# Optimization experiments

Hardware: AMD Instinct MI355X
Metric: run time of the kernel (lower is better)

Reference implementation:

```python
import jax, jax.numpy as jnp
import numpy as np

NEG_SLOPE = 0.2  # PyG GATConv leaky_relu slope
N_NODE = 1000   # nodes per graph (= n_nodes ctor arg = lstm1 input_size)
BATCH = 32      # num_graphs
C = 32          # in_channels == GAT out_channels per head
HEADS = 8
E = 384000      # total edges over the batched graph
H1, H2 = 32, 128
N_PRED = 2
N = N_NODE * BATCH


def _lstm(x_seq, W_ih, W_hh, b_ih, b_hh):
    # x_seq: [T, B, In]; PyTorch gate order i,f,g,o
    B = x_seq.shape[1]
    Hd = W_hh.shape[1]
    h0 = jnp.zeros((B, Hd), x_seq.dtype)

    def step(carry, x_t):
        h, c = carry
        g = x_t @ W_ih.T + h @ W_hh.T + b_ih + b_hh
        i, f, gg, o = jnp.split(g, 4, axis=-1)
        c = jax.nn.sigmoid(f) * c + jax.nn.sigmoid(i) * jnp.tanh(gg)
        h = jax.nn.sigmoid(o) * jnp.tanh(c)
        return (h, c), h

    (_, _), hs = jax.lax.scan(step, (h0, h0), x_seq)
    return hs


def setup_inputs() -> dict:
    key = jax.random.key(0)
    ks = jax.random.split(key, 20)
    inp = {}
    inp["x"] = jax.random.normal(ks[0], (N, C), jnp.float32)
    inp["src"] = jax.random.randint(ks[1], (E,), 0, N)
    inp["dst"] = jax.random.randint(ks[2], (E,), 0, N)
    inp["batch_size"] = BATCH
    # GATConv params (concat=False: mean over heads)
    inp["W_gat"] = jax.random.normal(ks[3], (C, HEADS * C), jnp.float32) * 0.1
    inp["a_src"] = jax.random.normal(ks[4], (HEADS, C), jnp.float32) * 0.1
    inp["a_dst"] = jax.random.normal(ks[5], (HEADS, C), jnp.float32) * 0.1
    inp["b_gat"] = jnp.zeros((C,), jnp.float32)
    # LSTM1: input N_NODE -> hidden 32
    inp["W_ih1"] = jax.random.normal(ks[6], (4 * H1, N_NODE), jnp.float32) * 0.05
    inp["W_hh1"] = jax.random.normal(ks[7], (4 * H1, H1), jnp.float32) * 0.1
    inp["b_ih1"] = jnp.zeros((4 * H1,), jnp.float32)
    inp["b_hh1"] = jnp.zeros((4 * H1,), jnp.float32)
    # LSTM2: input 32 -> hidden 128 (repaired from buggy source)
    inp["W_ih2"] = jax.random.normal(ks[8], (4 * H2, H1), jnp.float32) * 0.1
    inp["W_hh2"] = jax.random.normal(ks[9], (4 * H2, H2), jnp.float32) * 0.08
    inp["b_ih2"] = jnp.zeros((4 * H2,), jnp.float32)
    inp["b_hh2"] = jnp.zeros((4 * H2,), jnp.float32)
    # Linear head: 128 -> n_nodes * n_pred
    inp["W_lin"] = jax.random.normal(ks[10], (N_NODE * N_PRED, H2), jnp.float32) * 0.08
    inp["b_lin"] = jnp.zeros((N_NODE * N_PRED,), jnp.float32)
    return inp


def reference(x, src, dst, batch_size, W_gat, a_src, a_dst, b_gat,
              W_ih1, W_hh1, b_ih1, b_hh1, W_ih2, W_hh2, b_ih2, b_hh2,
              W_lin, b_lin):
    n, c = x.shape
    h = a_src.shape[0]
    # --- GATConv ---
    x_lin = (x @ W_gat).reshape(n, h, c)               # [N, H, C]
    asrc = jnp.einsum('nhc,hc->nh', x_lin, a_src)      # [N, H]
    adst = jnp.einsum('nhc,hc->nh', x_lin, a_dst)
    e = jax.nn.leaky_relu(asrc[src] + adst[dst], NEG_SLOPE)   # [E, H]
    m = jax.ops.segment_max(e, dst, num_segments=n)
    m = jnp.where(jnp.isfinite(m), m, 0.0)             # isolated nodes
    ew = jnp.exp(e - m[dst])
    denom = jax.ops.segment_sum(ew, dst, num_segments=n)
    alpha = ew / jnp.maximum(denom[dst], 1e-16)        # segment softmax
    agg = jax.ops.segment_sum(alpha[:, :, None] * x_lin[src], dst, num_segments=n)
    out = agg.mean(axis=1) + b_gat                     # concat=False -> head mean; [N, C]
    # --- reshape: seq over feature dim, LSTM input = nodes-per-graph ---
    n_node = n // batch_size
    seq = jnp.moveaxis(out.reshape(batch_size, n_node, c), 2, 0)  # [C, B, n_node]
    h1 = _lstm(seq, W_ih1, W_hh1, b_ih1, b_hh1)
    h2 = _lstm(h1, W_ih2, W_hh2, b_ih2, b_hh2)
    last = h2[-1]                                       # [B, 128]
    y = last @ W_lin.T + b_lin                          # [B, n_node*n_pred]
    return y.reshape(batch_size * n_node, -1)           # [B*n_node, n_pred]
```

## Files before the change

kernel.cpp:

```cpp
#include <hip/hip_runtime.h>
#include <hip/hip_fp16.h>
#include <math.h>

#define NEG_SLOPE 0.2f

__device__ __forceinline__ float sigm(float x) { return 1.0f / (1.0f + __expf(-x)); }
__device__ __forceinline__ float tanh_fast(float x) {
    float xc = fminf(fmaxf(x, -15.0f), 15.0f);
    float e2 = __expf(2.0f * xc);
    return (e2 - 1.0f) / (e2 + 1.0f);
}
__device__ __forceinline__ float lrelu(float x) { return (x > 0.0f) ? x : NEG_SLOPE * x; }

typedef _Float16 h2v __attribute__((ext_vector_type(2)));
__device__ __forceinline__ float fdot2h(h2v a, h2v b, float c) {
#if __has_builtin(__builtin_amdgcn_fdot2)
    return __builtin_amdgcn_fdot2(a, b, c, false);
#else
    return (float)a[0] * (float)b[0] + (float)a[1] * (float)b[1] + c;
#endif
}

__global__ void k_zero(int* __restrict__ deg, int N) {
    int i = blockIdx.x * 256 + threadIdx.x;
    if (i < N) deg[i] = 0;
}

__global__ void k_hist(const int* __restrict__ dst, int* __restrict__ deg, int E) {
    int e = blockIdx.x * 256 + threadIdx.x;
    if (e < E) atomicAdd(deg + dst[e], 1);
}

__global__ __launch_bounds__(256) void k_scan1(const int* __restrict__ deg,
                                               int* __restrict__ blksum, int N) {
    __shared__ int s[256];
    int tid = threadIdx.x;
    int i = blockIdx.x * 256 + tid;
    int v = (i < N) ? deg[i] : 0;
    s[tid] = v;
    __syncthreads();
    #pragma unroll
    for (int off = 128; off > 0; off >>= 1) {
        if (tid < off) s[tid] += s[tid + off];
        __syncthreads();
    }
    if (tid == 0) blksum[blockIdx.x] = s[0];
}

__global__ __launch_bounds__(256) void k_scan2(const int* __restrict__ blksum,
                                               int* __restrict__ blkoff, int nb) {
    __shared__ int s[256];
    int tid = threadIdx.x;
    int v = (tid < nb) ? blksum[tid] : 0;
    s[tid] = v;
    __syncthreads();
    for (int off = 1; off < 256; off <<= 1) {
        int t = (tid >= off) ? s[tid - off] : 0;
        __syncthreads();
        s[tid] += t;
        __syncthreads();
    }
    if (tid < nb) blkoff[tid] = s[tid] - v;
}

__global__ __launch_bounds__(256) void k_scan3(const int* __restrict__ deg,
                                               const int* __restrict__ blkoff,
                                               int* __restrict__ rowptr,
                                               int* __restrict__ cursor, int N, int E) {
    __shared__ int s[256];
    int tid = threadIdx.x;
    int i = blockIdx.x * 256 + tid;
    int v = (i < N) ? deg[i] : 0;
    s[tid] = v;
    __syncthreads();
    for (int off = 1; off < 256; off <<= 1) {
        int t = (tid >= off) ? s[tid - off] : 0;
        __syncthreads();
        s[tid] += t;
        __syncthreads();
    }
    int excl = s[tid] - v + blkoff[blockIdx.x];
    if (i < N) { rowptr[i] = excl; cursor[i] = excl; }
    if (i == N - 1) rowptr[N] = E;
}

__global__ void k_scatter(const int* __restrict__ src, const int* __restrict__ dst,
                          int* __restrict__ cursor, int* __restrict__ csr_src, int E) {
    int e = blockIdx.x * 256 + threadIdx.x;
    if (e < E) {
        int pos = atomicAdd(cursor + dst[e], 1);
        csr_src[pos] = src[e];
    }
}

__global__ void k_pre(const float* __restrict__ W_gat, const float* __restrict__ a_src,
                      const float* __restrict__ a_dst, float* __restrict__ wa) {
    int tid = threadIdx.x;
    int k = tid >> 3, h = tid & 7;
    float s1 = 0.0f, s2 = 0.0f;
    for (int c = 0; c < 32; ++c) {
        float wv = W_gat[k * 256 + h * 32 + c];
        s1 += wv * a_src[h * 32 + c];
        s2 += wv * a_dst[h * 32 + c];
    }
    wa[tid] = s1;
    wa[256 + tid] = s2;
}

__global__ __launch_bounds__(256) void k_att(const float* __restrict__ x,
                                             const float* __restrict__ wa,
                                             float* __restrict__ asrc,
                                             float* __restrict__ adst) {
    __shared__ float xs[32 * 33];
    __shared__ float was[256], wad[256];
    int tid = threadIdx.x;
    int n0 = blockIdx.x * 32;
    for (int i = tid; i < 1024; i += 256) {
        int nl = i >> 5, k = i & 31;
        xs[nl * 33 + k] = x[(size_t)(n0 + nl) * 32 + k];
    }
    was[tid] = wa[tid];
    wad[tid] = wa[256 + tid];
    __syncthreads();
    int nl = tid >> 3, h = tid & 7;
    float s1 = 0.0f, s2 = 0.0f;
    #pragma unroll
    for (int k = 0; k < 32; ++k) {
        float xv = xs[nl * 33 + k];
        s1 += xv * was[k * 8 + h];
        s2 += xv * wad[k * 8 + h];
    }
    asrc[(size_t)(n0 + nl) * 8 + h] = s1;
    adst[(size_t)(n0 + nl) * 8 + h] = s2;
}

__global__ __launch_bounds__(256) void k_gat(
    const int* __restrict__ rowptr, const int* __restrict__ csr_src,
    const float* __restrict__ asrc, const float* __restrict__ adst,
    const float* __restrict__ x, float* __restrict__ z, int N) {
    int w = (blockIdx.x * 256 + threadIdx.x) >> 6;
    int lane = threadIdx.x & 63;
    if (w >= N) return;
    int r0 = rowptr[w], r1 = rowptr[w + 1];
    int h = lane >> 3, kq = lane & 7;
    float ad = adst[w * 8 + h];
    float4 acc = make_float4(0.0f, 0.0f, 0.0f, 0.0f);
    float den = 0.0f;
    const float4* x4 = (const float4*)x;
    for (int i = r0; i < r1; ++i) {
        int s = csr_src[i];
        float ew = __expf(lrelu(asrc[s * 8 + h] + ad));
        float4 xv = x4[(size_t)s * 8 + kq];
        acc.x += ew * xv.x; acc.y += ew * xv.y;
        acc.z += ew * xv.z; acc.w += ew * xv.w;
        den += ew;
    }
    float inv = 1.0f / fmaxf(den, 1e-16f);
    float4 r = make_float4(acc.x * inv, acc.y * inv, acc.z * inv, acc.w * inv);
    ((float4*)z)[(size_t)w * 64 + lane] = r;
}

__global__ __launch_bounds__(256) void k_zw(
    const float* __restrict__ z, const float* __restrict__ W_gat,
    const float* __restrict__ b_gat, float* __restrict__ gatT, int N, int n_node) {
    int gw = (blockIdx.x * 256 + threadIdx.x) >> 6;
    int lane = threadIdx.x & 63;
    int chalf = gw & 1;
    int nset = gw >> 1;
    int c = chalf * 16 + (lane & 15);
    int sl = lane >> 4;
    float wcol[64];
    #pragma unroll
    for (int i = 0; i < 64; ++i) {
        int k = i & 31, hh = sl * 2 + (i >> 5);
        wcol[i] = 0.125f * W_gat[k * 256 + hh * 32 + c];
    }
    float bg = b_gat[c];
    const float4* z4 = (const float4*)z;
    for (int it = 0; it < 8; ++it) {
        int n = nset * 8 + it;
        if (n >= N) break;
        float p = 0.0f;
        #pragma unroll
        for (int k4 = 0; k4 < 16; ++k4) {
            float4 zv = z4[(size_t)n * 64 + sl * 16 + k4];
            p += zv.x * wcol[4 * k4] + zv.y * wcol[4 * k4 + 1]
               + zv.z * wcol[4 * k4 + 2] + zv.w * wcol[4 * k4 + 3];
        }
        p += __shfl_xor(p, 16, 64);
        p += __shfl_xor(p, 32, 64);
        if (lane < 16) {
            int b = n / n_node, kk = n - b * n_node;
            gatT[((size_t)b * 32 + c) * n_node + kk] = p + bg;
        }
    }
}

__global__ __launch_bounds__(256) void k_wt(const float* __restrict__ W,
                                            float* __restrict__ Wt, int n_node) {
    __shared__ float tle[32][33];
    int kt = blockIdx.x & 31;
    int gt = blockIdx.x >> 5;
    int tid = threadIdx.x;
    for (int i = tid; i < 1024; i += 256) {
        int gl = i >> 5, kl = i & 31;
        int g = gt * 32 + gl, k = kt * 32 + kl;
        tle[gl][kl] = (k < n_node) ? W[(size_t)g * n_node + k] : 0.0f;
    }
    __syncthreads();
    for (int i = tid; i < 1024; i += 256) {
        int kl = i >> 5, gl = i & 31;
        int k = kt * 32 + kl, g = gt * 32 + gl;
        if (k < n_node) Wt[(size_t)k * 128 + g] = tle[gl][kl];
    }
}

__global__ __launch_bounds__(256) void k_p1(
    const float* __restrict__ gatT, const float* __restrict__ Wt,
    const float* __restrict__ b_ih1, const float* __restrict__ b_hh1,
    float* __restrict__ P1, int n_node, int B) {
    __shared__ __align__(16) float Arow[2][1024];
    __shared__ __align__(16) float part[4][2][128];
    int blk = blockIdx.x;
    int b = blk >> 4;
    int tq = blk & 15;
    int tid = threadIdx.x;
    const float* A0 = gatT + ((size_t)b * 32 + tq * 2) * n_node;
    #pragma unroll
    for (int r = 0; r < 2; ++r)
        for (int i = tid; i < n_node; i += 256)
            Arow[r][i] = A0[(size_t)r * n_node + i];
    __syncthreads();

    int g4 = tid & 31;
    int tloc = (tid >> 5) & 1;
    int ks = tid >> 6;
    int kq = n_node >> 2;
    int k0 = ks * kq;
    const float4* Wt4 = (const float4*)Wt;
    float4 acc = make_float4(0.0f, 0.0f, 0.0f, 0.0f);
    #pragma unroll 4
    for (int k = 0; k < kq; ++k) {
        float4 w = Wt4[(size_t)(k0 + k) * 32 + g4];
        float a = Arow[tloc][k0 + k];
        acc.x += w.x * a; acc.y += w.y * a;
        acc.z += w.z * a; acc.w += w.w * a;
    }
    *(float4*)&part[ks][tloc][g4 * 4] = acc;
    __syncthreads();

    int tl = tid >> 7, g = tid & 127;
    float s = part[0][tl][g] + part[1][tl][g] + part[2][tl][g] + part[3][tl][g]
            + b_ih1[g] + b_hh1[g];
    int t = tq * 2 + tl;
    P1[((size_t)t * B + b) * 128 + g] = s;
}

__global__ __launch_bounds__(640) void k_lstm(
    const float* __restrict__ P1, const float* __restrict__ W_hh1,
    const float* __restrict__ W_ih2, const float* __restrict__ W_hh2,
    const float* __restrict__ b_ih2, const float* __restrict__ b_hh2,
    float* __restrict__ h2finT, int B, int T) {
    __shared__ __align__(16) float P1s[32][128];
    __shared__ __align__(16) float h1s[32];
    __shared__ __align__(16) float g1s[128];
    __shared__ __align__(16) float h1all[32][32];
    __shared__ __align__(16) __half hbuf[2][128];
    int tid = threadIdx.x, b = blockIdx.x;

    for (int i = tid; i < 4096; i += 640) {
        int t = i >> 7, g = i & 127;
        P1s[t][g] = P1[((size_t)t * B + b) * 128 + g];
    }

    float4 w1[8];
    if (tid < 128) {
        const float4* W = (const float4*)(W_hh1 + (size_t)tid * 32);
        #pragma unroll
        for (int j = 0; j < 8; ++j) w1[j] = W[j];
    }

    int tid2 = tid - 128;
    int gt = tid2 & 3, n = tid2 >> 2;
    int g_idx = gt * 128 + n;
    h2v wh[64];
    float4 wi[8];
    float bias = 0.0f;
    if (tid >= 128) {
        const float4* Wr = (const float4*)(W_hh2 + (size_t)g_idx * 128);
        #pragma unroll
        for (int j = 0; j < 32; ++j) {
            float4 w = Wr[j];
            h2v t0, t1;
            t0[0] = (_Float16)w.x; t0[1] = (_Float16)w.y;
            t1[0] = (_Float16)w.z; t1[1] = (_Float16)w.w;
            wh[2 * j] = t0;
            wh[2 * j + 1] = t1;
        }
        const float4* Wi = (const float4*)(W_ih2 + (size_t)g_idx * 32);
        #pragma unroll
        for (int j = 0; j < 8; ++j) wi[j] = Wi[j];
        bias = b_ih2[g_idx] + b_hh2[g_idx];
    }

    if (tid < 32) h1s[tid] = 0.0f;
    if (tid >= 128 && tid < 256) hbuf[0][tid - 128] = __float2half(0.0f);
    float c1 = 0.0f, c2 = 0.0f;
    __syncthreads();

    for (int s = 0; s <= T; ++s) {
        if (tid < 128) {
            if (s < T) {
                float acc = P1s[s][tid];
                const float4* hp = (const float4*)h1s;
                #pragma unroll
                for (int j = 0; j < 8; ++j) {
                    float4 h = hp[j], w = w1[j];
                    acc += w.x * h.x + w.y * h.y + w.z * h.z + w.w * h.w;
                }
                g1s[tid] = acc;
            }
        } else if (s >= 1) {
            int t2 = s - 1;
            const float4* hp1 = (const float4*)h1all[t2];
            float p = bias;
            #pragma unroll
            for (int j = 0; j < 8; ++j) {
                float4 w = wi[j], h = hp1[j];
                p += w.x * h.x + w.y * h.y + w.z * h.z + w.w * h.w;
            }
            const uint4* hc4 = (const uint4*)hbuf[t2 & 1];
            float a0 = 0.0f, a1 = 0.0f, a2 = 0.0f, a3 = 0.0f;
            #pragma unroll
            for (int j = 0; j < 16; ++j) {
                uint4 hv = hc4[j];
                const h2v* hp = reinterpret_cast<const h2v*>(&hv);
                a0 = fdot2h(wh[4 * j],     hp[0], a0);
                a1 = fdot2h(wh[4 * j + 1], hp[1], a1);
                a2 = fdot2h(wh[4 * j + 2], hp[2], a2);
                a3 = fdot2h(wh[4 * j + 3], hp[3], a3);
            }
            float acc = p + ((a0 + a1) + (a2 + a3));
            float v1 = __shfl_xor(acc, 1, 64);
            float v2 = __shfl_xor(acc, 2, 64);
            float v3 = __shfl_xor(acc, 3, 64);
            if (gt == 0) {
                float i_ = sigm(acc), f_ = sigm(v1);
                float g_ = tanh_fast(v2), o_ = sigm(v3);
                c2 = f_ * c2 + i_ * g_;
                float h = o_ * tanh_fast(c2);
                hbuf[(t2 + 1) & 1][n] = __float2half(h);
                if (t2 == T - 1) h2finT[n * 32 + b] = h;
            }
        }
        __syncthreads();
        if (tid < 32 && s < T) {
            float i_ = sigm(g1s[tid]), f_ = sigm(g1s[32 + tid]);
            float g_ = tanh_fast(g1s[64 + tid]), o_ = sigm(g1s[96 + tid]);
            c1 = f_ * c1 + i_ * g_;
            float h = o_ * tanh_fast(c1);
            h1s[tid] = h;
            h1all[s][tid] = h;
        }
        __syncthreads();
    }
}

__global__ __launch_bounds__(256) void k_fin(
    const float* __restrict__ h2finT, const float* __restrict__ W_lin,
    const float* __restrict__ b_lin, float* __restrict__ out, int n_node, int B) {
    __shared__ __align__(16) float hs[128];
    int b = blockIdx.x >> 3;
    int kc = blockIdx.x & 7;
    int tid = threadIdx.x;
    if (tid < 128) hs[tid] = h2finT[tid * 32 + b];
    __syncthreads();
    int outdim = n_node * 2;
    int kk = kc * 256 + tid;
    if (kk < outdim) {
        float acc = b_lin[kk];
        const float4* W4 = (const float4*)(W_lin + (size_t)kk * 128);
        const float4* h4 = (const float4*)hs;
        #pragma unroll 8
        for (int j = 0; j < 32; ++j) {
            float4 w = W4[j], h = h4[j];
            acc += w.x * h.x + w.y * h.y + w.z * h.z + w.w * h.w;
        }
        out[(size_t)b * outdim + kk] = acc;
    }
}

extern "C" void kernel_launch(void* const* d_in, const int* in_sizes, int n_in,
                              void* d_out, int out_size, void* d_ws, size_t ws_size,
                              hipStream_t stream) {
    const float* x     = (const float*)d_in[0];
    const int*   src   = (const int*)d_in[1];
    const int*   dst   = (const int*)d_in[2];
    const float* W_gat = (const float*)d_in[4];
    const float* a_src = (const float*)d_in[5];
    const float* a_dst = (const float*)d_in[6];
    const float* b_gat = (const float*)d_in[7];
    const float* W_ih1 = (const float*)d_in[8];
    const float* W_hh1 = (const float*)d_in[9];
    const float* b_ih1 = (const float*)d_in[10];
    const float* b_hh1 = (const float*)d_in[11];
    const float* W_ih2 = (const float*)d_in[12];
    const float* W_hh2 = (const float*)d_in[13];
    const float* b_ih2 = (const float*)d_in[14];
    const float* b_hh2 = (const float*)d_in[15];
    const float* W_lin = (const float*)d_in[16];
    const float* b_lin = (const float*)d_in[17];

    int N = in_sizes[0] / 32;
    int E = in_sizes[1];
    int n_node = in_sizes[8] / 128;
    int B = N / n_node;
    int T = 32;

    float* ws = (float*)d_ws;
    float* z      = ws;
    float* asrc   = z + (size_t)N * 256;
    float* adst   = asrc + (size_t)N * 8;
    float* gatT   = adst + (size_t)N * 8;
    float* P1     = gatT + (size_t)N * 32;
    float* h1g    = P1 + (size_t)T * B * 128;
    float* P2g    = h1g + (size_t)B * 1024;
    float* h2finT = P2g + (size_t)B * 16384;
    float* wa     = h2finT + 128 * 32;
    int* deg     = (int*)(wa + 512);
    int* cursor  = deg + N;
    int* rowptr  = cursor + N;
    int* csr_src = rowptr + N + 1;
    int* blksum  = csr_src + E;
    int* blkoff  = blksum + 256;
    float* Wt    = (float*)(((uintptr_t)(blkoff + 256) + 255) & ~(uintptr_t)255);

    int nb = (N + 255) / 256;

    k_wt<<<128, 256, 0, stream>>>(W_ih1, Wt, n_node);
    k_zero<<<(N + 255) / 256, 256, 0, stream>>>(deg, N);
    k_hist<<<(E + 255) / 256, 256, 0, stream>>>(dst, deg, E);
    k_scan1<<<nb, 256, 0, stream>>>(deg, blksum, N);
    k_scan2<<<1, 256, 0, stream>>>(blksum, blkoff, nb);
    k_scan3<<<nb, 256, 0, stream>>>(deg, blkoff, rowptr, cursor, N, E);
    k_scatter<<<(E + 255) / 256, 256, 0, stream>>>(src, dst, cursor, csr_src, E);
    k_pre<<<1, 256, 0, stream>>>(W_gat, a_src, a_dst, wa);
    k_att<<<N / 32, 256, 0, stream>>>(x, wa, asrc, adst);
    k_gat<<<(N * 64 + 255) / 256, 256, 0, stream>>>(rowptr, csr_src, asrc, adst,
                                                    x, z, N);
    k_zw<<<2000, 256, 0, stream>>>(z, W_gat, b_gat, gatT, N, n_node);
    k_p1<<<B * 16, 256, 0, stream>>>(gatT, Wt, b_ih1, b_hh1, P1, n_node, B);
    k_lstm<<<B, 640, 0, stream>>>(P1, W_hh1, W_ih2, W_hh2, b_ih2, b_hh2,
                                  h2finT, B, T);
    k_fin<<<B * 8, 256, 0, stream>>>(h2finT, W_lin, b_lin, (float*)d_out, n_node, B);
}
```

Measured before the change: 239.8 us.

## Fuse LSTM1 gate activation via shuffles, drop a barrier, prepack LSTM2 weights

Reorders LSTM1 gate rows so each group of four lanes holds the i/f/g/o gates of one hidden unit. The cell update is then done with lane shuffles instead of a shared-memory round trip, which removes one __syncthreads per time step and double-buffers h1. LSTM2 recurrent weights are converted to fp16 and packed in a coalesced layout by a new pre-kernel, so the LSTM kernel's weight loads are coalesced and need no conversion. The dot-product loop uses eight accumulators, and launch bounds now request 3 blocks per SM, which may constrain register allocation.

Result: faster. 228.3 us (-4.8%).

```diff
diff --git a/kernel.cpp b/kernel.cpp
--- a/kernel.cpp
+++ b/kernel.cpp
@@ -215,6 +215,23 @@
     }
 }
 
+__global__ __launch_bounds__(256) void k_pack2(
+    const float* __restrict__ W_hh2, const float* __restrict__ W_ih2,
+    uint4* __restrict__ wpack, float4* __restrict__ wipack) {
+    int i = blockIdx.x * 256 + threadIdx.x;
+    int j = i >> 9, t2 = i & 511;
+    int g = (t2 & 3) * 128 + (t2 >> 2);
+    const float* p = W_hh2 + (size_t)g * 128 + j * 8;
+    __align__(16) _Float16 tmp[8];
+    #pragma unroll
+    for (int k = 0; k < 8; ++k) tmp[k] = (_Float16)p[k];
+    wpack[j * 512 + t2] = *(const uint4*)tmp;
+    if (j < 8) {
+        const float4* q = (const float4*)(W_ih2 + (size_t)g * 32) + j;
+        wipack[j * 512 + t2] = *q;
+    }
+}
+
 __global__ __launch_bounds__(256) void k_p1(
     const float* __restrict__ gatT, const float* __restrict__ Wt,
     const float* __restrict__ b_ih1, const float* __restrict__ b_hh1,
@@ -256,14 +273,13 @@
     P1[((size_t)t * B + b) * 128 + g] = s;
 }
 
-__global__ __launch_bounds__(640) void k_lstm(
+__global__ __launch_bounds__(640, 3) void k_lstm(
     const float* __restrict__ P1, const float* __restrict__ W_hh1,
-    const float* __restrict__ W_ih2, const float* __restrict__ W_hh2,
+    const uint4* __restrict__ wpack, const float4* __restrict__ wipack,
     const float* __restrict__ b_ih2, const float* __restrict__ b_hh2,
     float* __restrict__ h2finT, int B, int T) {
     __shared__ __align__(16) float P1s[32][128];
-    __shared__ __align__(16) float h1s[32];
-    __shared__ __align__(16) float g1s[128];
+    __shared__ __align__(16) float h1d[2][32];
     __shared__ __align__(16) float h1all[32][32];
     __shared__ __align__(16) __half hbuf[2][128];
     int tid = threadIdx.x, b = blockIdx.x;
@@ -273,9 +289,12 @@
         P1s[t][g] = P1[((size_t)t * B + b) * 128 + g];
     }
 
+    int n1 = (tid >> 2) & 31, gt1 = tid & 3;
+    int r1 = gt1 * 32 + n1;
     float4 w1[8];
+    float c1 = 0.0f;
     if (tid < 128) {
-        const float4* W = (const float4*)(W_hh1 + (size_t)tid * 32);
+        const float4* W = (const float4*)(W_hh1 + (size_t)r1 * 32);
         #pragma unroll
         for (int j = 0; j < 8; ++j) w1[j] = W[j];
     }
@@ -283,64 +302,72 @@
     int tid2 = tid - 128;
     int gt = tid2 & 3, n = tid2 >> 2;
     int g_idx = gt * 128 + n;
-    h2v wh[64];
+    uint4 whq[16];
     float4 wi[8];
-    float bias = 0.0f;
+    float bias = 0.0f, c2 = 0.0f;
     if (tid >= 128) {
-        const float4* Wr = (const float4*)(W_hh2 + (size_t)g_idx * 128);
         #pragma unroll
-        for (int j = 0; j < 32; ++j) {
-            float4 w = Wr[j];
-            h2v t0, t1;
-            t0[0] = (_Float16)w.x; t0[1] = (_Float16)w.y;
-            t1[0] = (_Float16)w.z; t1[1] = (_Float16)w.w;
-            wh[2 * j] = t0;
-            wh[2 * j + 1] = t1;
-        }
-        const float4* Wi = (const float4*)(W_ih2 + (size_t)g_idx * 32);
+        for (int j = 0; j < 16; ++j) whq[j] = wpack[j * 512 + tid2];
         #pragma unroll
-        for (int j = 0; j < 8; ++j) wi[j] = Wi[j];
+        for (int j = 0; j < 8; ++j) wi[j] = wipack[j * 512 + tid2];
         bias = b_ih2[g_idx] + b_hh2[g_idx];
     }
 
-    if (tid < 32) h1s[tid] = 0.0f;
+    if (tid < 32) h1d[0][tid] = 0.0f;
     if (tid >= 128 && tid < 256) hbuf[0][tid - 128] = __float2half(0.0f);
-    float c1 = 0.0f, c2 = 0.0f;
     __syncthreads();
 
     for (int s = 0; s <= T; ++s) {
         if (tid < 128) {
             if (s < T) {
-                float acc = P1s[s][tid];
-                const float4* hp = (const float4*)h1s;
+                float acc = P1s[s][r1];
+                const float4* hp = (const float4*)h1d[s & 1];
                 #pragma unroll
                 for (int j = 0; j < 8; ++j) {
                     float4 h = hp[j], w = w1[j];
                     acc += w.x * h.x + w.y * h.y + w.z * h.z + w.w * h.w;
                 }
-                g1s[tid] = acc;
+                float v1 = __shfl_xor(acc, 1, 64);
+                float v2 = __shfl_xor(acc, 2, 64);
+                float v3 = __shfl_xor(acc, 3, 64);
+                if (gt1 == 0) {
+                    float i_ = sigm(acc), f_ = sigm(v1);
+                    float g_ = tanh_fast(v2), o_ = sigm(v3);
+                    c1 = f_ * c1 + i_ * g_;
+                    float h = o_ * tanh_fast(c1);
+                    h1d[(s + 1) & 1][n1] = h;
+                    h1all[s][n1] = h;
+                }
             }
         } else if (s >= 1) {
-            int t2 = s - 1;
-            const float4* hp1 = (const float4*)h1all[t2];
+            int t2s = s - 1;
+            const float4* hp1 = (const float4*)h1all[t2s];
             float p = bias;
             #pragma unroll
             for (int j = 0; j < 8; ++j) {
                 float4 w = wi[j], h = hp1[j];
                 p += w.x * h.x + w.y * h.y + w.z * h.z + w.w * h.w;
             }
-            const uint4* hc4 = (const uint4*)hbuf[t2 & 1];
+            const uint4* hc4 = (const uint4*)hbuf[t2s & 1];
             float a0 = 0.0f, a1 = 0.0f, a2 = 0.0f, a3 = 0.0f;
+            float a4 = 0.0f, a5 = 0.0f, a6 = 0.0f, a7 = 0.0f;
             #pragma unroll
-            for (int j = 0; j < 16; ++j) {
-                uint4 hv = hc4[j];
-                const h2v* hp = reinterpret_cast<const h2v*>(&hv);
-                a0 = fdot2h(wh[4 * j],     hp[0], a0);
-                a1 = fdot2h(wh[4 * j + 1], hp[1], a1);
-                a2 = fdot2h(wh[4 * j + 2], hp[2], a2);
-                a3 = fdot2h(wh[4 * j + 3], hp[3], a3);
+            for (int j = 0; j < 16; j += 2) {
+                uint4 hvA = hc4[j], hvB = hc4[j + 1];
+                const h2v* ha = reinterpret_cast<const h2v*>(&hvA);
+                const h2v* hb = reinterpret_cast<const h2v*>(&hvB);
+                const h2v* wa_ = reinterpret_cast<const h2v*>(&whq[j]);
+                const h2v* wb_ = reinterpret_cast<const h2v*>(&whq[j + 1]);
+                a0 = fdot2h(wa_[0], ha[0], a0);
+                a1 = fdot2h(wa_[1], ha[1], a1);
+                a2 = fdot2h(wa_[2], ha[2], a2);
+                a3 = fdot2h(wa_[3], ha[3], a3);
+                a4 = fdot2h(wb_[0], hb[0], a4);
+                a5 = fdot2h(wb_[1], hb[1], a5);
+                a6 = fdot2h(wb_[2], hb[2], a6);
+                a7 = fdot2h(wb_[3], hb[3], a7);
             }
-            float acc = p + ((a0 + a1) + (a2 + a3));
+            float acc = p + (((a0 + a1) + (a2 + a3)) + ((a4 + a5) + (a6 + a7)));
             float v1 = __shfl_xor(acc, 1, 64);
             float v2 = __shfl_xor(acc, 2, 64);
             float v3 = __shfl_xor(acc, 3, 64);
@@ -349,18 +376,9 @@
                 float g_ = tanh_fast(v2), o_ = sigm(v3);
                 c2 = f_ * c2 + i_ * g_;
                 float h = o_ * tanh_fast(c2);
-                hbuf[(t2 + 1) & 1][n] = __float2half(h);
-                if (t2 == T - 1) h2finT[n * 32 + b] = h;
+                hbuf[(t2s + 1) & 1][n] = __float2half(h);
+                if (t2s == T - 1) h2finT[n * 32 + b] = h;
             }
-        }
-        __syncthreads();
-        if (tid < 32 && s < T) {
-            float i_ = sigm(g1s[tid]), f_ = sigm(g1s[32 + tid]);
-            float g_ = tanh_fast(g1s[64 + tid]), o_ = sigm(g1s[96 + tid]);
-            c1 = f_ * c1 + i_ * g_;
-            float h = o_ * tanh_fast(c1);
-            h1s[tid] = h;
-            h1all[s][tid] = h;
         }
         __syncthreads();
     }
@@ -423,9 +441,9 @@
     float* adst   = asrc + (size_t)N * 8;
     float* gatT   = adst + (size_t)N * 8;
     float* P1     = gatT + (size_t)N * 32;
-    float* h1g    = P1 + (size_t)T * B * 128;
-    float* P2g    = h1g + (size_t)B * 1024;
-    float* h2finT = P2g + (size_t)B * 16384;
+    float* wpackf = P1 + (size_t)T * B * 128;
+    float* wipackf= wpackf + 32768;
+    float* h2finT = wipackf + 16384;
     float* wa     = h2finT + 128 * 32;
     int* deg     = (int*)(wa + 512);
     int* cursor  = deg + N;
@@ -435,8 +453,12 @@
     int* blkoff  = blksum + 256;
     float* Wt    = (float*)(((uintptr_t)(blkoff + 256) + 255) & ~(uintptr_t)255);
 
+    uint4*  wpack  = (uint4*)wpackf;
+    float4* wipack = (float4*)wipackf;
+
     int nb = (N + 255) / 256;
 
+    k_pack2<<<32, 256, 0, stream>>>(W_hh2, W_ih2, wpack, wipack);
     k_wt<<<128, 256, 0, stream>>>(W_ih1, Wt, n_node);
     k_zero<<<(N + 255) / 256, 256, 0, stream>>>(deg, N);
     k_hist<<<(E + 255) / 256, 256, 0, stream>>>(dst, deg, E);
@@ -450,7 +472,7 @@
                                                     x, z, N);
     k_zw<<<2000, 256, 0, stream>>>(z, W_gat, b_gat, gatT, N, n_node);
     k_p1<<<B * 16, 256, 0, stream>>>(gatT, Wt, b_ih1, b_hh1, P1, n_node, B);
-    k_lstm<<<B, 640, 0, stream>>>(P1, W_hh1, W_ih2, W_hh2, b_ih2, b_hh2,
+    k_lstm<<<B, 640, 0, stream>>>(P1, W_hh1, wpack, wipack, b_ih2, b_hh2,
                                   h2finT, B, T);
     k_fin<<<B * 8, 256, 0, stream>>>(h2finT, W_lin, b_lin, (float*)d_out, n_node, B);
 }
```

## Restructure fused LSTM kernel to 1024 threads with split-K gate dot products

Applied to the files above, without the earlier changes.

The fused two-layer LSTM kernel now uses 1024 threads per batch. Eight threads split each hidden unit's recurrent dot product and combine partial sums with shuffles, instead of one thread per gate holding a full fp16 weight row. A new pre-pack kernel converts and reorders W_hh2, W_ih2 and W_hh1 into coalesced per-thread layouts. Layer 1 now uses shuffles for its gates and double-buffered h1, which removes one barrier per timestep, and layer 2 runs concurrently one step behind. The aim is to shorten the serial per-step latency of the recurrence, at the cost of an extra launch and more shuffle work.

After: 240.7 us. About the same (+0.4%).

```diff
diff --git a/kernel.cpp b/kernel.cpp
--- a/kernel.cpp
+++ b/kernel.cpp
@@ -215,6 +215,33 @@
     }
 }
 
+__global__ __launch_bounds__(256) void k_pack2(
+    const float* __restrict__ W_hh2, const float* __restrict__ W_ih2,
+    const float* __restrict__ W_hh1,
+    uint4* __restrict__ wc2, float4* __restrict__ wif4, float4* __restrict__ w1f4) {
+    int i = blockIdx.x * 256 + threadIdx.x;
+    if (i < 8192) {
+        int j = i >> 10, t = i & 1023;
+        int n = t >> 3, q = t & 7;
+        int g = j >> 1, jj = j & 1;
+        const float* p = W_hh2 + (size_t)(g * 128 + n) * 128 + q * 16 + jj * 8;
+        __align__(16) _Float16 tmp[8];
+        #pragma unroll
+        for (int k = 0; k < 8; ++k) tmp[k] = (_Float16)p[k];
+        wc2[j * 1024 + t] = *(const uint4*)tmp;
+    } else if (i < 12288) {
+        int ii = i - 8192;
+        int j = ii >> 10, t = ii & 1023;
+        int n = t >> 3, q = t & 7;
+        wif4[j * 1024 + t] = *(const float4*)(W_ih2 + (size_t)(j * 128 + n) * 32 + q * 4);
+    } else if (i < 13312) {
+        int ii = i - 12288;
+        int j = ii >> 7, t1 = ii & 127;
+        int r1 = (t1 & 3) * 32 + (t1 >> 2);
+        w1f4[j * 128 + t1] = *(const float4*)(W_hh1 + (size_t)r1 * 32 + j * 4);
+    }
+}
+
 __global__ __launch_bounds__(256) void k_p1(
     const float* __restrict__ gatT, const float* __restrict__ Wt,
     const float* __restrict__ b_ih1, const float* __restrict__ b_hh1,
@@ -256,111 +283,129 @@
     P1[((size_t)t * B + b) * 128 + g] = s;
 }
 
-__global__ __launch_bounds__(640) void k_lstm(
-    const float* __restrict__ P1, const float* __restrict__ W_hh1,
-    const float* __restrict__ W_ih2, const float* __restrict__ W_hh2,
+__attribute__((amdgpu_waves_per_eu(4, 4)))
+__global__ __launch_bounds__(1024) void k_lstm(
+    const float* __restrict__ P1, const uint4* __restrict__ wc2,
+    const float4* __restrict__ wif4, const float4* __restrict__ w1f4,
     const float* __restrict__ b_ih2, const float* __restrict__ b_hh2,
     float* __restrict__ h2finT, int B, int T) {
     __shared__ __align__(16) float P1s[32][128];
-    __shared__ __align__(16) float h1s[32];
-    __shared__ __align__(16) float g1s[128];
-    __shared__ __align__(16) float h1all[32][32];
+    __shared__ __align__(16) float h1d[2][32];
     __shared__ __align__(16) __half hbuf[2][128];
     int tid = threadIdx.x, b = blockIdx.x;
-
-    for (int i = tid; i < 4096; i += 640) {
-        int t = i >> 7, g = i & 127;
-        P1s[t][g] = P1[((size_t)t * B + b) * 128 + g];
-    }
-
+    int n = tid >> 3, q = tid & 7;
+
+    for (int i = tid; i < 4096; i += 1024)
+        P1s[i >> 7][i & 127] = P1[((size_t)(i >> 7) * B + b) * 128 + (i & 127)];
+
+    uint4 wc[8];
+    #pragma unroll
+    for (int j = 0; j < 8; ++j) wc[j] = wc2[j * 1024 + tid];
+    float4 wi0 = wif4[tid];
+    float4 wi1 = wif4[1024 + tid];
+    float4 wi2 = wif4[2048 + tid];
+    float4 wi3 = wif4[3072 + tid];
+    float bias0 = b_ih2[n] + b_hh2[n];
+    float bias1 = b_ih2[128 + n] + b_hh2[128 + n];
+    float bias2 = b_ih2[256 + n] + b_hh2[256 + n];
+    float bias3 = b_ih2[384 + n] + b_hh2[384 + n];
+
+    int gt1 = tid & 3;
+    int r1 = gt1 * 32 + (tid >> 2);
     float4 w1[8];
     if (tid < 128) {
-        const float4* W = (const float4*)(W_hh1 + (size_t)tid * 32);
         #pragma unroll
-        for (int j = 0; j < 8; ++j) w1[j] = W[j];
-    }
-
-    int tid2 = tid - 128;
-    int gt = tid2 & 3, n = tid2 >> 2;
-    int g_idx = gt * 128 + n;
-    h2v wh[64];
-    float4 wi[8];
-    float bias = 0.0f;
-    if (tid >= 128) {
-        const float4* Wr = (const float4*)(W_hh2 + (size_t)g_idx * 128);
-        #pragma unroll
-        for (int j = 0; j < 32; ++j) {
-            float4 w = Wr[j];
-            h2v t0, t1;
-            t0[0] = (_Float16)w.x; t0[1] = (_Float16)w.y;
-            t1[0] = (_Float16)w.z; t1[1] = (_Float16)w.w;
-            wh[2 * j] = t0;
-            wh[2 * j + 1] = t1;
-        }
-        const float4* Wi = (const float4*)(W_ih2 + (size_t)g_idx * 32);
-        #pragma unroll
-        for (int j = 0; j < 8; ++j) wi[j] = Wi[j];
-        bias = b_ih2[g_idx] + b_hh2[g_idx];
-    }
-
-    if (tid < 32) h1s[tid] = 0.0f;
-    if (tid >= 128 && tid < 256) hbuf[0][tid - 128] = __float2half(0.0f);
+        for (int j = 0; j < 8; ++j) w1[j] = w1f4[j * 128 + tid];
+    }
+    if (tid < 32) h1d[0][tid] = 0.0f;
+    if (tid < 128) hbuf[0][tid] = __float2half(0.0f);
     float c1 = 0.0f, c2 = 0.0f;
     __syncthreads();
 
     for (int s = 0; s <= T; ++s) {
-        if (tid < 128) {
-            if (s < T) {
-                float acc = P1s[s][tid];
-                const float4* hp = (const float4*)h1s;
-                #pragma unroll
-                for (int j = 0; j < 8; ++j) {
-                    float4 h = hp[j], w = w1[j];
-                    acc += w.x * h.x + w.y * h.y + w.z * h.z + w.w * h.w;
-                }
-                g1s[tid] = acc;
-            }
-        } else if (s >= 1) {
+        if (s >= 1) {
             int t2 = s - 1;
-            const float4* hp1 = (const float4*)h1all[t2];
-            float p = bias;
-            #pragma unroll
-            for (int j = 0; j < 8; ++j) {
-                float4 w = wi[j], h = hp1[j];
-                p += w.x * h.x + w.y * h.y + w.z * h.z + w.w * h.w;
-            }
-            const uint4* hc4 = (const uint4*)hbuf[t2 & 1];
-            float a0 = 0.0f, a1 = 0.0f, a2 = 0.0f, a3 = 0.0f;
-            #pragma unroll
-            for (int j = 0; j < 16; ++j) {
-                uint4 hv = hc4[j];
-                const h2v* hp = reinterpret_cast<const h2v*>(&hv);
-                a0 = fdot2h(wh[4 * j],     hp[0], a0);
-                a1 = fdot2h(wh[4 * j + 1], hp[1], a1);
-                a2 = fdot2h(wh[4 * j + 2], hp[2], a2);
-                a3 = fdot2h(wh[4 * j + 3], hp[3], a3);
-            }
-            float acc = p + ((a0 + a1) + (a2 + a3));
-            float v1 = __shfl_xor(acc, 1, 64);
-            float v2 = __shfl_xor(acc, 2, 64);
-            float v3 = __shfl_xor(acc, 3, 64);
-            if (gt == 0) {
-                float i_ = sigm(acc), f_ = sigm(v1);
-                float g_ = tanh_fast(v2), o_ = sigm(v3);
+            const uint4* hb = (const uint4*)hbuf[t2 & 1];
+            uint4 h2a = hb[q * 2];
+            uint4 h2b = hb[q * 2 + 1];
+            float4 h1v = ((const float4*)h1d[s & 1])[q];
+            const h2v* ha = reinterpret_cast<const h2v*>(&h2a);
+            const h2v* hc = reinterpret_cast<const h2v*>(&h2b);
+            float sg0 = wi0.x * h1v.x + wi0.y * h1v.y + wi0.z * h1v.z + wi0.w * h1v.w;
+            float sg1 = wi1.x * h1v.x + wi1.y * h1v.y + wi1.z * h1v.z + wi1.w * h1v.w;
+            float sg2 = wi2.x * h1v.x + wi2.y * h1v.y + wi2.z * h1v.z + wi2.w * h1v.w;
+            float sg3 = wi3.x * h1v.x + wi3.y * h1v.y + wi3.z * h1v.z + wi3.w * h1v.w;
+            {
+                const h2v* wa_ = reinterpret_cast<const h2v*>(&wc[0]);
+                const h2v* wb_ = reinterpret_cast<const h2v*>(&wc[1]);
+                float a0 = 0, a1 = 0, a2 = 0, a3 = 0;
+                a0 = fdot2h(wa_[0], ha[0], a0); a1 = fdot2h(wa_[1], ha[1], a1);
+                a2 = fdot2h(wa_[2], ha[2], a2); a3 = fdot2h(wa_[3], ha[3], a3);
+                a0 = fdot2h(wb_[0], hc[0], a0); a1 = fdot2h(wb_[1], hc[1], a1);
+                a2 = fdot2h(wb_[2], hc[2], a2); a3 = fdot2h(wb_[3], hc[3], a3);
+                sg0 += (a0 + a1) + (a2 + a3);
+            }
+            {
+                const h2v* wa_ = reinterpret_cast<const h2v*>(&wc[2]);
+                const h2v* wb_ = reinterpret_cast<const h2v*>(&wc[3]);
+                float a0 = 0, a1 = 0, a2 = 0, a3 = 0;
+                a0 = fdot2h(wa_[0], ha[0], a0); a1 = fdot2h(wa_[1], ha[1], a1);
+                a2 = fdot2h(wa_[2], ha[2], a2); a3 = fdot2h(wa_[3], ha[3], a3);
+                a0 = fdot2h(wb_[0], hc[0], a0); a1 = fdot2h(wb_[1], hc[1], a1);
+                a2 = fdot2h(wb_[2], hc[2], a2); a3 = fdot2h(wb_[3], hc[3], a3);
+                sg1 += (a0 + a1) + (a2 + a3);
+            }
+            {
+                const h2v* wa_ = reinterpret_cast<const h2v*>(&wc[4]);
+                const h2v* wb_ = reinterpret_cast<const h2v*>(&wc[5]);
+                float a0 = 0, a1 = 0, a2 = 0, a3 = 0;
+                a0 = fdot2h(wa_[0], ha[0], a0); a1 = fdot2h(wa_[1], ha[1], a1);
+                a2 = fdot2h(wa_[2], ha[2], a2); a3 = fdot2h(wa_[3], ha[3], a3);
+                a0 = fdot2h(wb_[0], hc[0], a0); a1 = fdot2h(wb_[1], hc[1], a1);
+                a2 = fdot2h(wb_[2], hc[2], a2); a3 = fdot2h(wb_[3], hc[3], a3);
+                sg2 += (a0 + a1) + (a2 + a3);
+            }
+            {
+                const h2v* wa_ = reinterpret_cast<const h2v*>(&wc[6]);
+                const h2v* wb_ = reinterpret_cast<const h2v*>(&wc[7]);
+                float a0 = 0, a1 = 0, a2 = 0, a3 = 0;
+                a0 = fdot2h(wa_[0], ha[0], a0); a1 = fdot2h(wa_[1], ha[1], a1);
+                a2 = fdot2h(wa_[2], ha[2], a2); a3 = fdot2h(wa_[3], ha[3], a3);
+                a0 = fdot2h(wb_[0], hc[0], a0); a1 = fdot2h(wb_[1], hc[1], a1);
+                a2 = fdot2h(wb_[2], hc[2], a2); a3 = fdot2h(wb_[3], hc[3], a3);
+                sg3 += (a0 + a1) + (a2 + a3);
+            }
+            sg0 += __shfl_xor(sg0, 1, 64); sg0 += __shfl_xor(sg0, 2, 64); sg0 += __shfl_xor(sg0, 4, 64);
+            sg1 += __shfl_xor(sg1, 1, 64); sg1 += __shfl_xor(sg1, 2, 64); sg1 += __shfl_xor(sg1, 4, 64);
+            sg2 += __shfl_xor(sg2, 1, 64); sg2 += __shfl_xor(sg2, 2, 64); sg2 += __shfl_xor(sg2, 4, 64);
+            sg3 += __shfl_xor(sg3, 1, 64); sg3 += __shfl_xor(sg3, 2, 64); sg3 += __shfl_xor(sg3, 4, 64);
+            if (q == 0) {
+                float i_ = sigm(sg0 + bias0), f_ = sigm(sg1 + bias1);
+                float g_ = tanh_fast(sg2 + bias2), o_ = sigm(sg3 + bias3);
                 c2 = f_ * c2 + i_ * g_;
                 float h = o_ * tanh_fast(c2);
                 hbuf[(t2 + 1) & 1][n] = __float2half(h);
                 if (t2 == T - 1) h2finT[n * 32 + b] = h;
             }
         }
-        __syncthreads();
-        if (tid < 32 && s < T) {
-            float i_ = sigm(g1s[tid]), f_ = sigm(g1s[32 + tid]);
-            float g_ = tanh_fast(g1s[64 + tid]), o_ = sigm(g1s[96 + tid]);
-            c1 = f_ * c1 + i_ * g_;
-            float h = o_ * tanh_fast(c1);
-            h1s[tid] = h;
-            h1all[s][tid] = h;
+        if (tid < 128 && s < T) {
+            const float4* hp = (const float4*)h1d[s & 1];
+            float acc = P1s[s][r1];
+            #pragma unroll
+            for (int j = 0; j < 8; ++j) {
+                float4 h = hp[j], w = w1[j];
+                acc += w.x * h.x + w.y * h.y + w.z * h.z + w.w * h.w;
+            }
+            float v1 = __shfl_xor(acc, 1, 64);
+            float v2 = __shfl_xor(acc, 2, 64);
+            float v3 = __shfl_xor(acc, 3, 64);
+            if (gt1 == 0) {
+                float i_ = sigm(acc), f_ = sigm(v1);
+                float g_ = tanh_fast(v2), o_ = sigm(v3);
+                c1 = f_ * c1 + i_ * g_;
+                float h = o_ * tanh_fast(c1);
+                h1d[(s + 1) & 1][tid >> 2] = h;
+            }
         }
         __syncthreads();
     }
@@ -423,9 +468,10 @@
     float* adst   = asrc + (size_t)N * 8;
     float* gatT   = adst + (size_t)N * 8;
     float* P1     = gatT + (size_t)N * 32;
-    float* h1g    = P1 + (size_t)T * B * 128;
-    float* P2g    = h1g + (size_t)B * 1024;
-    float* h2finT = P2g + (size_t)B * 16384;
+    float* wc2f   = P1 + (size_t)T * B * 128;
+    float* wiff   = wc2f + 32768;
+    float* w1ff   = wiff + 16384;
+    float* h2finT = w1ff + 4096;
     float* wa     = h2finT + 128 * 32;
     int* deg     = (int*)(wa + 512);
     int* cursor  = deg + N;
@@ -435,8 +481,13 @@
     int* blkoff  = blksum + 256;
     float* Wt    = (float*)(((uintptr_t)(blkoff + 256) + 255) & ~(uintptr_t)255);
 
+    uint4*  wc2  = (uint4*)wc2f;
+    float4* wif4 = (float4*)wiff;
+    float4* w1f4 = (float4*)w1ff;
+
     int nb = (N + 255) / 256;
 
+    k_pack2<<<52, 256, 0, stream>>>(W_hh2, W_ih2, W_hh1, wc2, wif4, w1f4);
     k_wt<<<128, 256, 0, stream>>>(W_ih1, Wt, n_node);
     k_zero<<<(N + 255) / 256, 256, 0, stream>>>(deg, N);
     k_hist<<<(E + 255) / 256, 256, 0, stream>>>(dst, deg, E);
@@ -450,7 +501,6 @@
                                                     x, z, N);
     k_zw<<<2000, 256, 0, stream>>>(z, W_gat, b_gat, gatT, N, n_node);
     k_p1<<<B * 16, 256, 0, stream>>>(gatT, Wt, b_ih1, b_hh1, P1, n_node, B);
-    k_lstm<<<B, 640, 0, stream>>>(P1, W_hh1, W_ih2, W_hh2, b_ih2, b_hh2,
-                                  h2finT, B, T);
+    k_lstm<<<B, 1024, 0, stream>>>(P1, wc2, wif4, w1f4, b_ih2, b_hh2, h2finT, B, T);
     k_fin<<<B * 8, 256, 0, stream>>>(h2finT, W_lin, b_lin, (float*)d_out, n_node, B);
 }
```

## Restructure fused LSTM kernel to 256 threads with prepacked fp16 weights

Applied to the files above, without the earlier changes.

Adds a packing kernel that converts W_hh2, W_ih2 and W_hh1 to fp16 in a thread-coalesced layout. The LSTM kernel is rewritten to use 256 threads, each computing two gate rows for one hidden unit, with gates exchanged via lane shuffles instead of shared memory. LSTM1 gates are also computed and combined inside one wavefront, which removes one barrier per timestep. The aim is to shorten the serial recurrence latency by cutting barriers and thread count. The cost is an extra launch and fp16 precision for h1 and the input weights.

Result: faster. 220.6 us (-8.0%).

```diff
diff --git a/kernel.cpp b/kernel.cpp
--- a/kernel.cpp
+++ b/kernel.cpp
@@ -19,6 +19,16 @@
 #else
     return (float)a[0] * (float)b[0] + (float)a[1] * (float)b[1] + c;
 #endif
+}
+
+__device__ __forceinline__ float dot16(const uint4& w, const uint4& h, float acc) {
+    const h2v* wp = reinterpret_cast<const h2v*>(&w);
+    const h2v* hp = reinterpret_cast<const h2v*>(&h);
+    acc = fdot2h(wp[0], hp[0], acc);
+    acc = fdot2h(wp[1], hp[1], acc);
+    acc = fdot2h(wp[2], hp[2], acc);
+    acc = fdot2h(wp[3], hp[3], acc);
+    return acc;
 }
 
 __global__ void k_zero(int* __restrict__ deg, int N) {
@@ -215,6 +225,41 @@
     }
 }
 
+__global__ __launch_bounds__(256) void k_pack2(
+    const float* __restrict__ W_hh2, const float* __restrict__ W_ih2,
+    const float* __restrict__ W_hh1,
+    uint4* __restrict__ wc2p, uint4* __restrict__ wi2p, uint4* __restrict__ w1p) {
+    int i = blockIdx.x * 256 + threadIdx.x;
+    __align__(16) _Float16 tmp[8];
+    if (i < 8192) {
+        int jj = i >> 8, t = i & 255;
+        int p = jj >> 4, j = jj & 15;
+        int r = (t & 1) * 256 + p * 128 + (t >> 1);
+        const float* s = W_hh2 + (size_t)r * 128 + j * 8;
+        #pragma unroll
+        for (int k = 0; k < 8; ++k) tmp[k] = (_Float16)s[k];
+        wc2p[jj * 256 + t] = *(const uint4*)tmp;
+    } else if (i < 10240) {
+        int ii = i - 8192;
+        int jj = ii >> 8, t = ii & 255;
+        int p = jj >> 2, j = jj & 3;
+        int r = (t & 1) * 256 + p * 128 + (t >> 1);
+        const float* s = W_ih2 + (size_t)r * 32 + j * 8;
+        #pragma unroll
+        for (int k = 0; k < 8; ++k) tmp[k] = (_Float16)s[k];
+        wi2p[jj * 256 + t] = *(const uint4*)tmp;
+    } else if (i < 10752) {
+        int ii = i - 10240;
+        int jj = ii >> 6, l = ii & 63;
+        int p = jj >> 2, j = jj & 3;
+        int r = p * 64 + l;
+        const float* s = W_hh1 + (size_t)r * 32 + j * 8;
+        #pragma unroll
+        for (int k = 0; k < 8; ++k) tmp[k] = (_Float16)s[k];
+        w1p[jj * 64 + l] = *(const uint4*)tmp;
+    }
+}
+
 __global__ __launch_bounds__(256) void k_p1(
     const float* __restrict__ gatT, const float* __restrict__ Wt,
     const float* __restrict__ b_ih1, const float* __restrict__ b_hh1,
@@ -256,111 +301,98 @@
     P1[((size_t)t * B + b) * 128 + g] = s;
 }
 
-__global__ __launch_bounds__(640) void k_lstm(
-    const float* __restrict__ P1, const float* __restrict__ W_hh1,
-    const float* __restrict__ W_ih2, const float* __restrict__ W_hh2,
+__global__ __launch_bounds__(256, 1) void k_lstm(
+    const float* __restrict__ P1, const uint4* __restrict__ wc2p,
+    const uint4* __restrict__ wi2p, const uint4* __restrict__ w1p,
     const float* __restrict__ b_ih2, const float* __restrict__ b_hh2,
     float* __restrict__ h2finT, int B, int T) {
     __shared__ __align__(16) float P1s[32][128];
-    __shared__ __align__(16) float h1s[32];
-    __shared__ __align__(16) float g1s[128];
-    __shared__ __align__(16) float h1all[32][32];
-    __shared__ __align__(16) __half hbuf[2][128];
-    int tid = threadIdx.x, b = blockIdx.x;
-
-    for (int i = tid; i < 4096; i += 640) {
-        int t = i >> 7, g = i & 127;
-        P1s[t][g] = P1[((size_t)t * B + b) * 128 + g];
-    }
-
-    float4 w1[8];
-    if (tid < 128) {
-        const float4* W = (const float4*)(W_hh1 + (size_t)tid * 32);
+    __shared__ __align__(16) __half h1buf[2][32];
+    __shared__ __align__(16) __half h2buf[2][128];
+    int t = threadIdx.x, b = blockIdx.x;
+    int u = t >> 1, ht = t & 1;
+
+    for (int i = t; i < 1024; i += 256) {
+        int tt = i >> 5, c4 = i & 31;
+        ((float4*)P1s[tt])[c4] = ((const float4*)(P1 + ((size_t)tt * B + b) * 128))[c4];
+    }
+    uint4 wc[32];
+    #pragma unroll
+    for (int j = 0; j < 32; ++j) wc[j] = wc2p[j * 256 + t];
+    uint4 wi[8];
+    #pragma unroll
+    for (int j = 0; j < 8; ++j) wi[j] = wi2p[j * 256 + t];
+    uint4 w1[8];
+    if (t < 64) {
         #pragma unroll
-        for (int j = 0; j < 8; ++j) w1[j] = W[j];
-    }
-
-    int tid2 = tid - 128;
-    int gt = tid2 & 3, n = tid2 >> 2;
-    int g_idx = gt * 128 + n;
-    h2v wh[64];
-    float4 wi[8];
-    float bias = 0.0f;
-    if (tid >= 128) {
-        const float4* Wr = (const float4*)(W_hh2 + (size_t)g_idx * 128);
-        #pragma unroll
-        for (int j = 0; j < 32; ++j) {
-            float4 w = Wr[j];
-            h2v t0, t1;
-            t0[0] = (_Float16)w.x; t0[1] = (_Float16)w.y;
-            t1[0] = (_Float16)w.z; t1[1] = (_Float16)w.w;
-            wh[2 * j] = t0;
-            wh[2 * j + 1] = t1;
-        }
-        const float4* Wi = (const float4*)(W_ih2 + (size_t)g_idx * 32);
-        #pragma unroll
-        for (int j = 0; j < 8; ++j) wi[j] = Wi[j];
-        bias = b_ih2[g_idx] + b_hh2[g_idx];
-    }
-
-    if (tid < 32) h1s[tid] = 0.0f;
-    if (tid >= 128 && tid < 256) hbuf[0][tid - 128] = __float2half(0.0f);
+        for (int j = 0; j < 8; ++j) w1[j] = w1p[j * 64 + t];
+    }
+    int r0 = ht * 256 + u;
+    int r1 = ht * 256 + 128 + u;
+    float bias0 = b_ih2[r0] + b_hh2[r0];
+    float bias1 = b_ih2[r1] + b_hh2[r1];
+
+    if (t < 32) h1buf[0][t] = __float2half(0.0f);
+    if (t < 128) h2buf[0][t] = __float2half(0.0f);
     float c1 = 0.0f, c2 = 0.0f;
     __syncthreads();
 
     for (int s = 0; s <= T; ++s) {
-        if (tid < 128) {
-            if (s < T) {
-                float acc = P1s[s][tid];
-                const float4* hp = (const float4*)h1s;
-                #pragma unroll
-                for (int j = 0; j < 8; ++j) {
-                    float4 h = hp[j], w = w1[j];
-                    acc += w.x * h.x + w.y * h.y + w.z * h.z + w.w * h.w;
-                }
-                g1s[tid] = acc;
+        const uint4* h1q = (const uint4*)h1buf[s & 1];
+        uint4 hv0 = h1q[0], hv1 = h1q[1], hv2 = h1q[2], hv3 = h1q[3];
+
+        if (s >= 1) {
+            int t2 = s - 1;
+            const uint4* hb = (const uint4*)h2buf[t2 & 1];
+            float p0a, p0b, p1a, p1b;
+            p0a = dot16(wi[0], hv0, 0.0f); p0b = dot16(wi[1], hv1, 0.0f);
+            p0a = dot16(wi[2], hv2, p0a);  p0b = dot16(wi[3], hv3, p0b);
+            p1a = dot16(wi[4], hv0, 0.0f); p1b = dot16(wi[5], hv1, 0.0f);
+            p1a = dot16(wi[6], hv2, p1a);  p1b = dot16(wi[7], hv3, p1b);
+            #pragma unroll
+            for (int c = 0; c < 4; ++c) {
+                uint4 h0 = hb[c * 4], h1_ = hb[c * 4 + 1];
+                uint4 h2_ = hb[c * 4 + 2], h3 = hb[c * 4 + 3];
+                p0a = dot16(wc[c * 4], h0, p0a);
+                p0b = dot16(wc[c * 4 + 1], h1_, p0b);
+                p0a = dot16(wc[c * 4 + 2], h2_, p0a);
+                p0b = dot16(wc[c * 4 + 3], h3, p0b);
+                p1a = dot16(wc[16 + c * 4], h0, p1a);
+                p1b = dot16(wc[16 + c * 4 + 1], h1_, p1b);
+                p1a = dot16(wc[16 + c * 4 + 2], h2_, p1a);
+                p1b = dot16(wc[16 + c * 4 + 3], h3, p1b);
             }
-        } else if (s >= 1) {
-            int t2 = s - 1;
-            const float4* hp1 = (const float4*)h1all[t2];
-            float p = bias;
-            #pragma unroll
-            for (int j = 0; j < 8; ++j) {
-                float4 w = wi[j], h = hp1[j];
-                p += w.x * h.x + w.y * h.y + w.z * h.z + w.w * h.w;
-            }
-            const uint4* hc4 = (const uint4*)hbuf[t2 & 1];
-            float a0 = 0.0f, a1 = 0.0f, a2 = 0.0f, a3 = 0.0f;
-            #pragma unroll
-            for (int j = 0; j < 16; ++j) {
-                uint4 hv = hc4[j];
-                const h2v* hp = reinterpret_cast<const h2v*>(&hv);
-                a0 = fdot2h(wh[4 * j],     hp[0], a0);
-                a1 = fdot2h(wh[4 * j + 1], hp[1], a1);
-                a2 = fdot2h(wh[4 * j + 2], hp[2], a2);
-                a3 = fdot2h(wh[4 * j + 3], hp[3], a3);
-            }
-            float acc = p + ((a0 + a1) + (a2 + a3));
-            float v1 = __shfl_xor(acc, 1, 64);
-            float v2 = __shfl_xor(acc, 2, 64);
-            float v3 = __shfl_xor(acc, 3, 64);
-            if (gt == 0) {
-                float i_ = sigm(acc), f_ = sigm(v1);
-                float g_ = tanh_fast(v2), o_ = sigm(v3);
-                c2 = f_ * c2 + i_ * g_;
-                float h = o_ * tanh_fast(c2);
-                hbuf[(t2 + 1) & 1][n] = __float2half(h);
-                if (t2 == T - 1) h2finT[n * 32 + b] = h;
+            float s0 = p0a + p0b + bias0;
+            float s1 = p1a + p1b + bias1;
+            float o0 = __shfl_xor(s0, 1, 64);
+            float o1 = __shfl_xor(s1, 1, 64);
+            float gi = (ht == 0) ? s0 : o0;
+            float gf = (ht == 0) ? s1 : o1;
+            float gg = (ht == 0) ? o0 : s0;
+            float go = (ht == 0) ? o1 : s1;
+            c2 = sigm(gf) * c2 + sigm(gi) * tanh_fast(gg);
+            float h = sigm(go) * tanh_fast(c2);
+            if (ht == 0) {
+                h2buf[(t2 + 1) & 1][u] = __float2half(h);
+                if (t2 == T - 1) h2finT[u * 32 + b] = h;
             }
         }
-        __syncthreads();
-        if (tid < 32 && s < T) {
-            float i_ = sigm(g1s[tid]), f_ = sigm(g1s[32 + tid]);
-            float g_ = tanh_fast(g1s[64 + tid]), o_ = sigm(g1s[96 + tid]);
-            c1 = f_ * c1 + i_ * g_;
-            float h = o_ * tanh_fast(c1);
-            h1s[tid] = h;
-            h1all[s][tid] = h;
+        if (t < 64 && s < T) {
+            float aA = P1s[s][t];
+            float aB = P1s[s][64 + t];
+            aA = dot16(w1[0], hv0, aA); aA = dot16(w1[1], hv1, aA);
+            aA = dot16(w1[2], hv2, aA); aA = dot16(w1[3], hv3, aA);
+            aB = dot16(w1[4], hv0, aB); aB = dot16(w1[5], hv1, aB);
+            aB = dot16(w1[6], hv2, aB); aB = dot16(w1[7], hv3, aB);
+            float oA = __shfl_xor(aA, 32, 64);
+            float oB = __shfl_xor(aB, 32, 64);
+            float gi = (t < 32) ? aA : oA;
+            float gf = (t < 32) ? oA : aA;
+            float gg = (t < 32) ? aB : oB;
+            float go = (t < 32) ? oB : aB;
+            c1 = sigm(gf) * c1 + sigm(gi) * tanh_fast(gg);
+            float h = sigm(go) * tanh_fast(c1);
+            if (t < 32) h1buf[(s + 1) & 1][t] = __float2half(h);
         }
         __syncthreads();
     }
@@ -423,9 +455,10 @@
     float* adst   = asrc + (size_t)N * 8;
     float* gatT   = adst + (size_t)N * 8;
     float* P1     = gatT + (size_t)N * 32;
-    float* h1g    = P1 + (size_t)T * B * 128;
-    float* P2g    = h1g + (size_t)B * 1024;
-    float* h2finT = P2g + (size_t)B * 16384;
+    float* wc2f   = P1 + (size_t)T * B * 128;
+    float* wiff   = wc2f + 32768;
+    float* w1ff   = wiff + 8192;
+    float* h2finT = w1ff + 2048;
     float* wa     = h2finT + 128 * 32;
     int* deg     = (int*)(wa + 512);
     int* cursor  = deg + N;
@@ -435,8 +468,13 @@
     int* blkoff  = blksum + 256;
     float* Wt    = (float*)(((uintptr_t)(blkoff + 256) + 255) & ~(uintptr_t)255);
 
+    uint4* wc2p = (uint4*)wc2f;
+    uint4* wi2p = (uint4*)wiff;
+    uint4* w1p  = (uint4*)w1ff;
+
     int nb = (N + 255) / 256;
 
+    k_pack2<<<42, 256, 0, stream>>>(W_hh2, W_ih2, W_hh1, wc2p, wi2p, w1p);
     k_wt<<<128, 256, 0, stream>>>(W_ih1, Wt, n_node);
     k_zero<<<(N + 255) / 256, 256, 0, stream>>>(deg, N);
     k_hist<<<(E + 255) / 256, 256, 0, stream>>>(dst, deg, E);
@@ -450,7 +488,6 @@
                                                     x, z, N);
     k_zw<<<2000, 256, 0, stream>>>(z, W_gat, b_gat, gatT, N, n_node);
     k_p1<<<B * 16, 256, 0, stream>>>(gatT, Wt, b_ih1, b_hh1, P1, n_node, B);
-    k_lstm<<<B, 640, 0, stream>>>(P1, W_hh1, W_ih2, W_hh2, b_ih2, b_hh2,
-                                  h2finT, B, T);
+    k_lstm<<<B, 256, 0, stream>>>(P1, wc2p, wi2p, w1p, b_ih2, b_hh2, h2finT, B, T);
     k_fin<<<B * 8, 256, 0, stream>>>(h2finT, W_lin, b_lin, (float*)d_out, n_node, B);
 }
```
